# Kernel optimization log

Measured on AMD Instinct MI355X. Metric: run time of the kernel, lower is better.

## Reference

```python
import jax, jax.numpy as jnp
import numpy as np

H = 16  # num_heads

def setup_inputs() -> dict:
    key = jax.random.key(0)
    ks = jax.random.split(key, 9)
    B, S, D = 4, 1024, 1024
    s = 0.02
    return {
        "x": jax.random.normal(ks[0], (B, S, D), jnp.float32),
        "Wq": jax.random.normal(ks[1], (D, D), jnp.float32) * s,
        "bq": jax.random.normal(ks[2], (D,), jnp.float32) * s,
        "Wk": jax.random.normal(ks[3], (D, D), jnp.float32) * s,
        "bk": jax.random.normal(ks[4], (D,), jnp.float32) * s,
        "Wv": jax.random.normal(ks[5], (D, D), jnp.float32) * s,
        "bv": jax.random.normal(ks[6], (D,), jnp.float32) * s,
        "Wo": jax.random.normal(ks[7], (D, D), jnp.float32) * s,
        "bo": jax.random.normal(ks[8], (D,), jnp.float32) * s,
    }

def reference(x, Wq, bq, Wk, bk, Wv, bv, Wo, bo):
    B, S, D = x.shape
    hd = D // H
    # Batched equivalent of the per-head Linear loop: project then split into heads.
    def proj(W, b):
        return (x @ W + b).reshape(B, S, H, hd).transpose(0, 2, 1, 3)  # [B,H,S,hd]
    q, k, v = proj(Wq, bq), proj(Wk, bk), proj(Wv, bv)
    scores = jnp.einsum("bhqd,bhkd->bhqk", q, k) / jnp.sqrt(jnp.float32(hd))
    probs = jax.nn.softmax(scores, axis=-1)  # [B,H,S,S] (dropout p=0 -> identity)
    ctx = jnp.einsum("bhqk,bhkd->bhqd", probs, v)  # [B,H,S,hd]
    ctx = ctx.transpose(0, 2, 1, 3).reshape(B, S, D)  # concat heads
    out = ctx @ Wo + bo
    return out, probs
```

## Files before the change

### kernel.cpp

```cpp
#include <hip/hip_runtime.h>
#include <math.h>

typedef unsigned short u16;
typedef __attribute__((ext_vector_type(8))) short short8;
typedef __attribute__((ext_vector_type(4))) float f32x4;

#define BB 4
#define SS 1024
#define DD 1024
#define NH 16
#define HD 64
#define BH 64

__device__ __forceinline__ u16 f2bf(float f) {
    union { float f; unsigned u; } v;
    v.f = f;
    unsigned r = v.u + 0x7fffu + ((v.u >> 16) & 1u);
    return (u16)(r >> 16);
}

__global__ void cast_bf16(const float* __restrict__ X, u16* __restrict__ Y) {
    const int i = blockIdx.x * blockDim.x + threadIdx.x;
    const float4 v = reinterpret_cast<const float4*>(X)[i];
    ushort4 o;
    o.x = f2bf(v.x); o.y = f2bf(v.y); o.z = f2bf(v.z); o.w = f2bf(v.w);
    reinterpret_cast<ushort4*>(Y)[i] = o;
}

__global__ void transpose_cast_w(const float* __restrict__ W0, const float* __restrict__ W1,
                                 const float* __restrict__ W2, const float* __restrict__ W3,
                                 u16* __restrict__ O0, u16* __restrict__ O1,
                                 u16* __restrict__ O2, u16* __restrict__ O3) {
    __shared__ float T[64][65];
    const int z = blockIdx.z;
    const float* W = (z == 0) ? W0 : (z == 1) ? W1 : (z == 2) ? W2 : W3;
    u16* O = (z == 0) ? O0 : (z == 1) ? O1 : (z == 2) ? O2 : O3;
    const int k0 = blockIdx.x * 64, n0 = blockIdx.y * 64;
    const int x = threadIdx.x & 63, yq = threadIdx.x >> 6;
#pragma unroll
    for (int r = 0; r < 16; r++) {
        const int row = yq * 16 + r;
        T[row][x] = W[(size_t)(k0 + row) * 1024 + n0 + x];
    }
    __syncthreads();
#pragma unroll
    for (int r = 0; r < 16; r++) {
        const int row = yq * 16 + r;
        O[(size_t)(n0 + row) * 1024 + k0 + x] = f2bf(T[x][row]);
    }
}

__global__ void transpose_v(const u16* __restrict__ V, u16* __restrict__ VT) {
    __shared__ u16 T[64][66];
    const int t0 = blockIdx.x * 64;
    const size_t hbase = (size_t)blockIdx.y * (SS * HD);
    const int x = threadIdx.x & 63, yq = threadIdx.x >> 6;
#pragma unroll
    for (int r = 0; r < 16; r++) {
        const int trow = yq * 16 + r;
        T[trow][x] = V[hbase + (size_t)(t0 + trow) * 64 + x];
    }
    __syncthreads();
#pragma unroll
    for (int r = 0; r < 16; r++) {
        const int drow = yq * 16 + r;
        VT[hbase + (size_t)drow * 1024 + t0 + x] = T[x][drow];
    }
}

template <int MODE, int QKV>
__global__ __launch_bounds__(256) void mfma_gemm(
    const u16* __restrict__ A,
    const u16* __restrict__ Bt0, const u16* __restrict__ Bt1, const u16* __restrict__ Bt2,
    const float* __restrict__ bias0, const float* __restrict__ bias1, const float* __restrict__ bias2,
    void* __restrict__ out0, void* __restrict__ out1, void* __restrict__ out2) {
    __shared__ __align__(16) u16 As[128][32];
    __shared__ __align__(16) u16 Bs[128][32];

    const u16* Bt = Bt0;
    const float* bias = bias0;
    void* out = out0;
    if (QKV) {
        const int z = blockIdx.z;
        Bt = (z == 0) ? Bt0 : (z == 1) ? Bt1 : Bt2;
        bias = (z == 0) ? bias0 : (z == 1) ? bias1 : bias2;
        out = (z == 0) ? out0 : (z == 1) ? out1 : out2;
    }

    const int tid = threadIdx.x;
    const int w = tid >> 6, lane = tid & 63, l15 = lane & 15, quad = lane >> 4;
    const int wr = w >> 1, wc = w & 1;
    const int m0 = blockIdx.y * 128, n0 = blockIdx.x * 128;

    f32x4 acc[4][4];
#pragma unroll
    for (int i = 0; i < 4; i++)
#pragma unroll
        for (int j = 0; j < 4; j++) acc[i][j] = (f32x4){0.f, 0.f, 0.f, 0.f};

    for (int k0 = 0; k0 < 1024; k0 += 32) {
#pragma unroll
        for (int i = 0; i < 2; i++) {
            const int c = i * 256 + tid;
            const int row = c >> 2, in4 = c & 3;
            *(uint4*)(&As[row][in4 * 8]) =
                *(const uint4*)(A + (size_t)(m0 + row) * 1024 + k0 + in4 * 8);
            *(uint4*)(&Bs[row][in4 * 8]) =
                *(const uint4*)(Bt + (size_t)(n0 + row) * 1024 + k0 + in4 * 8);
        }
        __syncthreads();
        short8 af[4], bf[4];
#pragma unroll
        for (int i = 0; i < 4; i++)
            af[i] = *(const short8*)(&As[wr * 64 + i * 16 + l15][quad * 8]);
#pragma unroll
        for (int j = 0; j < 4; j++)
            bf[j] = *(const short8*)(&Bs[wc * 64 + j * 16 + l15][quad * 8]);
#pragma unroll
        for (int i = 0; i < 4; i++)
#pragma unroll
            for (int j = 0; j < 4; j++)
                acc[i][j] = __builtin_amdgcn_mfma_f32_16x16x32_bf16(af[i], bf[j], acc[i][j], 0, 0, 0);
        __syncthreads();
    }

#pragma unroll
    for (int i = 0; i < 4; i++) {
#pragma unroll
        for (int j = 0; j < 4; j++) {
            const int nn = n0 + wc * 64 + j * 16 + l15;
            const float bb = bias[nn];
#pragma unroll
            for (int r = 0; r < 4; r++) {
                const int mm = m0 + wr * 64 + i * 16 + quad * 4 + r;
                const float val = acc[i][j][r] + bb;
                if (MODE == 0) {
                    const int b = mm >> 10, s = mm & 1023, h = nn >> 6, d = nn & 63;
                    ((u16*)out)[((size_t)(b * NH + h) * SS + s) * HD + d] = f2bf(val);
                } else {
                    ((float*)out)[(size_t)mm * 1024 + nn] = val;
                }
            }
        }
    }
}

__global__ __launch_bounds__(256) void attn_fused(
    const u16* __restrict__ Qg, const u16* __restrict__ Kg, const u16* __restrict__ VTg,
    float* __restrict__ probs, u16* __restrict__ ctx) {
    __shared__ __align__(16) u16 Qs[2][64][32];
    __shared__ __align__(16) u16 Ks[2][64][32];
    __shared__ __align__(16) u16 Vs[2][64][32];
    __shared__ __align__(16) u16 Ps[4][2][16][32];

    const int tid = threadIdx.x;
    const int w = tid >> 6, lane = tid & 63, l15 = lane & 15, quad = lane >> 4;
    const int s0 = blockIdx.x * 64;
    const int bh = blockIdx.y;
    const size_t hbase = (size_t)bh * (SS * HD);

#pragma unroll
    for (int i = 0; i < 2; i++) {
        const int c = i * 256 + tid;
        const int row = c >> 3, ch = c & 7;
        *(uint4*)(&Qs[ch >> 2][row][(ch & 3) * 8]) =
            *(const uint4*)(Qg + hbase + (size_t)(s0 + row) * 64 + ch * 8);
    }

    float m_i[4], l_i[4];
#pragma unroll
    for (int r = 0; r < 4; r++) { m_i[r] = -1e30f; l_i[r] = 0.f; }

#pragma unroll 1
    for (int kt = 0; kt < 16; kt++) {
#pragma unroll
        for (int i = 0; i < 2; i++) {
            const int c = i * 256 + tid;
            const int row = c >> 3, ch = c & 7;
            *(uint4*)(&Ks[ch >> 2][row][(ch & 3) * 8]) =
                *(const uint4*)(Kg + hbase + (size_t)(kt * 64 + row) * 64 + ch * 8);
        }
        __syncthreads();
        const short8 aq0 = *(const short8*)(&Qs[0][w * 16 + l15][quad * 8]);
        const short8 aq1 = *(const short8*)(&Qs[1][w * 16 + l15][quad * 8]);
        f32x4 sc[4];
#pragma unroll
        for (int c = 0; c < 4; c++) {
            const short8 bk0 = *(const short8*)(&Ks[0][c * 16 + l15][quad * 8]);
            const short8 bk1 = *(const short8*)(&Ks[1][c * 16 + l15][quad * 8]);
            f32x4 z = {0.f, 0.f, 0.f, 0.f};
            z = __builtin_amdgcn_mfma_f32_16x16x32_bf16(aq0, bk0, z, 0, 0, 0);
            z = __builtin_amdgcn_mfma_f32_16x16x32_bf16(aq1, bk1, z, 0, 0, 0);
            sc[c] = z;
        }
#pragma unroll
        for (int r = 0; r < 4; r++) {
            float v = fmaxf(fmaxf(sc[0][r], sc[1][r]), fmaxf(sc[2][r], sc[3][r])) * 0.125f;
            v = fmaxf(v, __shfl_xor(v, 1));
            v = fmaxf(v, __shfl_xor(v, 2));
            v = fmaxf(v, __shfl_xor(v, 4));
            v = fmaxf(v, __shfl_xor(v, 8));
            const float mn = fmaxf(m_i[r], v);
            float ss = 0.f;
#pragma unroll
            for (int c = 0; c < 4; c++) ss += __expf(sc[c][r] * 0.125f - mn);
            ss += __shfl_xor(ss, 1);
            ss += __shfl_xor(ss, 2);
            ss += __shfl_xor(ss, 4);
            ss += __shfl_xor(ss, 8);
            l_i[r] = l_i[r] * __expf(m_i[r] - mn) + ss;
            m_i[r] = mn;
        }
        __syncthreads();
    }

    float linv[4];
#pragma unroll
    for (int r = 0; r < 4; r++) linv[r] = 1.0f / l_i[r];

    f32x4 oacc[4];
#pragma unroll
    for (int j = 0; j < 4; j++) oacc[j] = (f32x4){0.f, 0.f, 0.f, 0.f};

#pragma unroll 1
    for (int kt = 0; kt < 16; kt++) {
#pragma unroll
        for (int i = 0; i < 2; i++) {
            const int c = i * 256 + tid;
            const int row = c >> 3, ch = c & 7;
            *(uint4*)(&Ks[ch >> 2][row][(ch & 3) * 8]) =
                *(const uint4*)(Kg + hbase + (size_t)(kt * 64 + row) * 64 + ch * 8);
            *(uint4*)(&Vs[ch >> 2][row][(ch & 3) * 8]) =
                *(const uint4*)(VTg + hbase + (size_t)row * 1024 + kt * 64 + ch * 8);
        }
        __syncthreads();
        const short8 aq0 = *(const short8*)(&Qs[0][w * 16 + l15][quad * 8]);
        const short8 aq1 = *(const short8*)(&Qs[1][w * 16 + l15][quad * 8]);
        f32x4 sc[4];
#pragma unroll
        for (int c = 0; c < 4; c++) {
            const short8 bk0 = *(const short8*)(&Ks[0][c * 16 + l15][quad * 8]);
            const short8 bk1 = *(const short8*)(&Ks[1][c * 16 + l15][quad * 8]);
            f32x4 z = {0.f, 0.f, 0.f, 0.f};
            z = __builtin_amdgcn_mfma_f32_16x16x32_bf16(aq0, bk0, z, 0, 0, 0);
            z = __builtin_amdgcn_mfma_f32_16x16x32_bf16(aq1, bk1, z, 0, 0, 0);
            sc[c] = z;
        }
        const int qrow = s0 + w * 16 + quad * 4;
#pragma unroll
        for (int c = 0; c < 4; c++) {
            const int t = kt * 64 + c * 16 + l15;
#pragma unroll
            for (int r = 0; r < 4; r++) {
                const float p = __expf(sc[c][r] * 0.125f - m_i[r]) * linv[r];
                probs[((size_t)bh * SS + (qrow + r)) * SS + t] = p;
                Ps[w][c >> 1][quad * 4 + r][(c & 1) * 16 + l15] = f2bf(p);
            }
        }
        const short8 ap0 = *(const short8*)(&Ps[w][0][l15][quad * 8]);
        const short8 ap1 = *(const short8*)(&Ps[w][1][l15][quad * 8]);
#pragma unroll
        for (int j = 0; j < 4; j++) {
            const short8 bv0 = *(const short8*)(&Vs[0][j * 16 + l15][quad * 8]);
            const short8 bv1 = *(const short8*)(&Vs[1][j * 16 + l15][quad * 8]);
            oacc[j] = __builtin_amdgcn_mfma_f32_16x16x32_bf16(ap0, bv0, oacc[j], 0, 0, 0);
            oacc[j] = __builtin_amdgcn_mfma_f32_16x16x32_bf16(ap1, bv1, oacc[j], 0, 0, 0);
        }
        __syncthreads();
    }

    const int b = bh >> 4, h = bh & 15;
#pragma unroll
    for (int j = 0; j < 4; j++)
#pragma unroll
        for (int r = 0; r < 4; r++) {
            const int s = s0 + w * 16 + quad * 4 + r;
            ctx[((size_t)b * SS + s) * DD + h * HD + j * 16 + l15] = f2bf(oacc[j][r]);
        }
}

extern "C" void kernel_launch(void* const* d_in, const int* in_sizes, int n_in,
                              void* d_out, int out_size, void* d_ws, size_t ws_size,
                              hipStream_t stream) {
    const float* x  = (const float*)d_in[0];
    const float* Wq = (const float*)d_in[1];
    const float* bq = (const float*)d_in[2];
    const float* Wk = (const float*)d_in[3];
    const float* bk = (const float*)d_in[4];
    const float* Wv = (const float*)d_in[5];
    const float* bv = (const float*)d_in[6];
    const float* Wo = (const float*)d_in[7];
    const float* bo = (const float*)d_in[8];

    float* out   = (float*)d_out;
    float* probs = out + (size_t)BB * SS * DD;

    char* ws = (char*)d_ws;
    u16* xb   = (u16*)(ws);
    u16* Wtq  = (u16*)(ws + (8ull << 20));
    u16* Wtk  = (u16*)(ws + (10ull << 20));
    u16* Wtv  = (u16*)(ws + (12ull << 20));
    u16* Wto  = (u16*)(ws + (14ull << 20));
    u16* qb   = (u16*)(ws + (16ull << 20));
    u16* kb   = (u16*)(ws + (24ull << 20));
    u16* vb   = (u16*)(ws + (32ull << 20));
    u16* vTb  = (u16*)(ws + (40ull << 20));
    u16* ctxb = (u16*)(ws + (48ull << 20));

    const dim3 blk(256);

    cast_bf16<<<dim3(4096), blk, 0, stream>>>(x, xb);
    transpose_cast_w<<<dim3(16, 16, 4), blk, 0, stream>>>(Wq, Wk, Wv, Wo, Wtq, Wtk, Wtv, Wto);

    mfma_gemm<0, 1><<<dim3(8, 32, 3), blk, 0, stream>>>(
        xb, Wtq, Wtk, Wtv, bq, bk, bv, qb, kb, vb);

    transpose_v<<<dim3(16, 64), blk, 0, stream>>>(vb, vTb);

    attn_fused<<<dim3(16, 64), blk, 0, stream>>>(qb, kb, vTb, probs, ctxb);

    mfma_gemm<1, 0><<<dim3(8, 32), blk, 0, stream>>>(
        ctxb, Wto, nullptr, nullptr, bo, nullptr, nullptr, out, nullptr, nullptr);
}
```

Before: 470.2 us.

## Use direct global-to-LDS loads and transposed score layout for vectorized prob stores

The projection GEMM now uses global_load_lds to stream A and B tiles straight into LDS, with the K step doubled to 64 and two MFMA k-slices per step. The attention kernel swaps the MFMA operand order (K as A, Q as B) so each lane owns one query row. That lets the softmax reductions use cross-quad shuffles only and lets probs be written as contiguous float4 stores. The first pass reads K straight from global memory without LDS or barriers, and Q is kept in registers instead of LDS. The aim is to cut LDS staging, barriers and the cost of scattered scalar probability writes, at the risk of uncoalesced K reads in pass one and LDS layout mismatches from global_load_lds.

```diff
diff --git a/kernel.cpp b/kernel.cpp
--- a/kernel.cpp
+++ b/kernel.cpp
@@ -17,6 +17,11 @@
     v.f = f;
     unsigned r = v.u + 0x7fffu + ((v.u >> 16) & 1u);
     return (u16)(r >> 16);
+}
+
+__device__ __forceinline__ void gll16(const void* g, void* l) {
+    __builtin_amdgcn_global_load_lds((__attribute__((address_space(1))) void*)g,
+                                     (__attribute__((address_space(3))) void*)l, 16, 0, 0);
 }
 
 __global__ void cast_bf16(const float* __restrict__ X, u16* __restrict__ Y) {
@@ -74,8 +79,8 @@
     const u16* __restrict__ Bt0, const u16* __restrict__ Bt1, const u16* __restrict__ Bt2,
     const float* __restrict__ bias0, const float* __restrict__ bias1, const float* __restrict__ bias2,
     void* __restrict__ out0, void* __restrict__ out1, void* __restrict__ out2) {
-    __shared__ __align__(16) u16 As[128][32];
-    __shared__ __align__(16) u16 Bs[128][32];
+    __shared__ __align__(16) u16 As[128][64];
+    __shared__ __align__(16) u16 Bs[128][64];
 
     const u16* Bt = Bt0;
     const float* bias = bias0;
@@ -92,35 +97,40 @@
     const int wr = w >> 1, wc = w & 1;
     const int m0 = blockIdx.y * 128, n0 = blockIdx.x * 128;
 
+    const int srow = tid >> 3, sch = tid & 7;
+    const u16* Ag = A + (size_t)(m0 + srow) * 1024 + sch * 8;
+    const u16* Bg = Bt + (size_t)(n0 + srow) * 1024 + sch * 8;
+
     f32x4 acc[4][4];
 #pragma unroll
     for (int i = 0; i < 4; i++)
 #pragma unroll
         for (int j = 0; j < 4; j++) acc[i][j] = (f32x4){0.f, 0.f, 0.f, 0.f};
 
-    for (int k0 = 0; k0 < 1024; k0 += 32) {
-#pragma unroll
-        for (int i = 0; i < 2; i++) {
-            const int c = i * 256 + tid;
-            const int row = c >> 2, in4 = c & 3;
-            *(uint4*)(&As[row][in4 * 8]) =
-                *(const uint4*)(A + (size_t)(m0 + row) * 1024 + k0 + in4 * 8);
-            *(uint4*)(&Bs[row][in4 * 8]) =
-                *(const uint4*)(Bt + (size_t)(n0 + row) * 1024 + k0 + in4 * 8);
+    for (int k0 = 0; k0 < 1024; k0 += 64) {
+#pragma unroll
+        for (int i = 0; i < 4; i++) {
+            gll16(Ag + (size_t)(i * 32) * 1024 + k0, &As[i * 32 + w * 8][0]);
+            gll16(Bg + (size_t)(i * 32) * 1024 + k0, &Bs[i * 32 + w * 8][0]);
         }
         __syncthreads();
-        short8 af[4], bf[4];
+        short8 af[2][4], bf[2][4];
+#pragma unroll
+        for (int ks = 0; ks < 2; ks++) {
+#pragma unroll
+            for (int i = 0; i < 4; i++)
+                af[ks][i] = *(const short8*)(&As[wr * 64 + i * 16 + l15][ks * 32 + quad * 8]);
+#pragma unroll
+            for (int j = 0; j < 4; j++)
+                bf[ks][j] = *(const short8*)(&Bs[wc * 64 + j * 16 + l15][ks * 32 + quad * 8]);
+        }
 #pragma unroll
         for (int i = 0; i < 4; i++)
-            af[i] = *(const short8*)(&As[wr * 64 + i * 16 + l15][quad * 8]);
-#pragma unroll
-        for (int j = 0; j < 4; j++)
-            bf[j] = *(const short8*)(&Bs[wc * 64 + j * 16 + l15][quad * 8]);
-#pragma unroll
-        for (int i = 0; i < 4; i++)
-#pragma unroll
-            for (int j = 0; j < 4; j++)
-                acc[i][j] = __builtin_amdgcn_mfma_f32_16x16x32_bf16(af[i], bf[j], acc[i][j], 0, 0, 0);
+#pragma unroll
+            for (int j = 0; j < 4; j++) {
+                acc[i][j] = __builtin_amdgcn_mfma_f32_16x16x32_bf16(af[0][i], bf[0][j], acc[i][j], 0, 0, 0);
+                acc[i][j] = __builtin_amdgcn_mfma_f32_16x16x32_bf16(af[1][i], bf[1][j], acc[i][j], 0, 0, 0);
+            }
         __syncthreads();
     }
 
@@ -148,7 +158,6 @@
 __global__ __launch_bounds__(256) void attn_fused(
     const u16* __restrict__ Qg, const u16* __restrict__ Kg, const u16* __restrict__ VTg,
     float* __restrict__ probs, u16* __restrict__ ctx) {
-    __shared__ __align__(16) u16 Qs[2][64][32];
     __shared__ __align__(16) u16 Ks[2][64][32];
     __shared__ __align__(16) u16 Vs[2][64][32];
     __shared__ __align__(16) u16 Ps[4][2][16][32];
@@ -159,103 +168,91 @@
     const int bh = blockIdx.y;
     const size_t hbase = (size_t)bh * (SS * HD);
 
-#pragma unroll
-    for (int i = 0; i < 2; i++) {
-        const int c = i * 256 + tid;
-        const int row = c >> 3, ch = c & 7;
-        *(uint4*)(&Qs[ch >> 2][row][(ch & 3) * 8]) =
-            *(const uint4*)(Qg + hbase + (size_t)(s0 + row) * 64 + ch * 8);
-    }
-
-    float m_i[4], l_i[4];
-#pragma unroll
-    for (int r = 0; r < 4; r++) { m_i[r] = -1e30f; l_i[r] = 0.f; }
-
+    const int qg = s0 + w * 16 + l15;
+    const short8 bq0 = *(const short8*)(Qg + hbase + (size_t)qg * 64 + quad * 8);
+    const short8 bq1 = *(const short8*)(Qg + hbase + (size_t)qg * 64 + 32 + quad * 8);
+
+    float m_i = -1e30f, l_i = 0.f;
 #pragma unroll 1
     for (int kt = 0; kt < 16; kt++) {
+        f32x4 sc[4];
+#pragma unroll
+        for (int c = 0; c < 4; c++) {
+            const u16* kr = Kg + hbase + (size_t)(kt * 64 + c * 16 + l15) * 64 + quad * 8;
+            const short8 ak0 = *(const short8*)kr;
+            const short8 ak1 = *(const short8*)(kr + 32);
+            f32x4 z = {0.f, 0.f, 0.f, 0.f};
+            z = __builtin_amdgcn_mfma_f32_16x16x32_bf16(ak0, bq0, z, 0, 0, 0);
+            z = __builtin_amdgcn_mfma_f32_16x16x32_bf16(ak1, bq1, z, 0, 0, 0);
+            sc[c] = z;
+        }
+        float vm = -1e30f;
+#pragma unroll
+        for (int c = 0; c < 4; c++)
+#pragma unroll
+            for (int r = 0; r < 4; r++) {
+                sc[c][r] *= 0.125f;
+                vm = fmaxf(vm, sc[c][r]);
+            }
+        vm = fmaxf(vm, __shfl_xor(vm, 16));
+        vm = fmaxf(vm, __shfl_xor(vm, 32));
+        const float mn = fmaxf(m_i, vm);
+        float ss = 0.f;
+#pragma unroll
+        for (int c = 0; c < 4; c++)
+#pragma unroll
+            for (int r = 0; r < 4; r++) ss += __expf(sc[c][r] - mn);
+        ss += __shfl_xor(ss, 16);
+        ss += __shfl_xor(ss, 32);
+        l_i = l_i * __expf(m_i - mn) + ss;
+        m_i = mn;
+    }
+    const float linv = 1.0f / l_i;
+
+    f32x4 oacc[4];
+#pragma unroll
+    for (int j = 0; j < 4; j++) oacc[j] = (f32x4){0.f, 0.f, 0.f, 0.f};
+
+    const size_t prow = ((size_t)bh * SS + qg) * SS;
+
+#pragma unroll 1
+    for (int kt = 0; kt < 16; kt++) {
 #pragma unroll
         for (int i = 0; i < 2; i++) {
             const int c = i * 256 + tid;
-            const int row = c >> 3, ch = c & 7;
-            *(uint4*)(&Ks[ch >> 2][row][(ch & 3) * 8]) =
-                *(const uint4*)(Kg + hbase + (size_t)(kt * 64 + row) * 64 + ch * 8);
+            const int ks = c >> 8, row = (c >> 2) & 63, ch = c & 3;
+            const int cb = i * 256 + (tid & ~63);
+            gll16(Kg + hbase + (size_t)(kt * 64 + row) * 64 + ks * 32 + ch * 8,
+                  &Ks[0][0][0] + (size_t)cb * 8);
+            gll16(VTg + hbase + (size_t)row * 1024 + kt * 64 + ks * 32 + ch * 8,
+                  &Vs[0][0][0] + (size_t)cb * 8);
         }
         __syncthreads();
-        const short8 aq0 = *(const short8*)(&Qs[0][w * 16 + l15][quad * 8]);
-        const short8 aq1 = *(const short8*)(&Qs[1][w * 16 + l15][quad * 8]);
+
         f32x4 sc[4];
 #pragma unroll
         for (int c = 0; c < 4; c++) {
-            const short8 bk0 = *(const short8*)(&Ks[0][c * 16 + l15][quad * 8]);
-            const short8 bk1 = *(const short8*)(&Ks[1][c * 16 + l15][quad * 8]);
+            const short8 ak0 = *(const short8*)(&Ks[0][c * 16 + l15][quad * 8]);
+            const short8 ak1 = *(const short8*)(&Ks[1][c * 16 + l15][quad * 8]);
             f32x4 z = {0.f, 0.f, 0.f, 0.f};
-            z = __builtin_amdgcn_mfma_f32_16x16x32_bf16(aq0, bk0, z, 0, 0, 0);
-            z = __builtin_amdgcn_mfma_f32_16x16x32_bf16(aq1, bk1, z, 0, 0, 0);
+            z = __builtin_amdgcn_mfma_f32_16x16x32_bf16(ak0, bq0, z, 0, 0, 0);
+            z = __builtin_amdgcn_mfma_f32_16x16x32_bf16(ak1, bq1, z, 0, 0, 0);
             sc[c] = z;
         }
 #pragma unroll
-        for (int r = 0; r < 4; r++) {
-            float v = fmaxf(fmaxf(sc[0][r], sc[1][r]), fmaxf(sc[2][r], sc[3][r])) * 0.125f;
-            v = fmaxf(v, __shfl_xor(v, 1));
-            v = fmaxf(v, __shfl_xor(v, 2));
-            v = fmaxf(v, __shfl_xor(v, 4));
-            v = fmaxf(v, __shfl_xor(v, 8));
-            const float mn = fmaxf(m_i[r], v);
-            float ss = 0.f;
-#pragma unroll
-            for (int c = 0; c < 4; c++) ss += __expf(sc[c][r] * 0.125f - mn);
-            ss += __shfl_xor(ss, 1);
-            ss += __shfl_xor(ss, 2);
-            ss += __shfl_xor(ss, 4);
-            ss += __shfl_xor(ss, 8);
-            l_i[r] = l_i[r] * __expf(m_i[r] - mn) + ss;
-            m_i[r] = mn;
-        }
-        __syncthreads();
-    }
-
-    float linv[4];
-#pragma unroll
-    for (int r = 0; r < 4; r++) linv[r] = 1.0f / l_i[r];
-
-    f32x4 oacc[4];
-#pragma unroll
-    for (int j = 0; j < 4; j++) oacc[j] = (f32x4){0.f, 0.f, 0.f, 0.f};
-
-#pragma unroll 1
-    for (int kt = 0; kt < 16; kt++) {
-#pragma unroll
-        for (int i = 0; i < 2; i++) {
-            const int c = i * 256 + tid;
-            const int row = c >> 3, ch = c & 7;
-            *(uint4*)(&Ks[ch >> 2][row][(ch & 3) * 8]) =
-                *(const uint4*)(Kg + hbase + (size_t)(kt * 64 + row) * 64 + ch * 8);
-            *(uint4*)(&Vs[ch >> 2][row][(ch & 3) * 8]) =
-                *(const uint4*)(VTg + hbase + (size_t)row * 1024 + kt * 64 + ch * 8);
-        }
-        __syncthreads();
-        const short8 aq0 = *(const short8*)(&Qs[0][w * 16 + l15][quad * 8]);
-        const short8 aq1 = *(const short8*)(&Qs[1][w * 16 + l15][quad * 8]);
-        f32x4 sc[4];
-#pragma unroll
         for (int c = 0; c < 4; c++) {
-            const short8 bk0 = *(const short8*)(&Ks[0][c * 16 + l15][quad * 8]);
-            const short8 bk1 = *(const short8*)(&Ks[1][c * 16 + l15][quad * 8]);
-            f32x4 z = {0.f, 0.f, 0.f, 0.f};
-            z = __builtin_amdgcn_mfma_f32_16x16x32_bf16(aq0, bk0, z, 0, 0, 0);
-            z = __builtin_amdgcn_mfma_f32_16x16x32_bf16(aq1, bk1, z, 0, 0, 0);
-            sc[c] = z;
-        }
-        const int qrow = s0 + w * 16 + quad * 4;
-#pragma unroll
-        for (int c = 0; c < 4; c++) {
-            const int t = kt * 64 + c * 16 + l15;
+            float p[4];
+            f32x4 pv;
 #pragma unroll
             for (int r = 0; r < 4; r++) {
-                const float p = __expf(sc[c][r] * 0.125f - m_i[r]) * linv[r];
-                probs[((size_t)bh * SS + (qrow + r)) * SS + t] = p;
-                Ps[w][c >> 1][quad * 4 + r][(c & 1) * 16 + l15] = f2bf(p);
+                p[r] = __expf(sc[c][r] * 0.125f - m_i) * linv;
+                pv[r] = p[r];
             }
+            *(f32x4*)(probs + prow + kt * 64 + c * 16 + quad * 4) = pv;
+            uint2 pk;
+            pk.x = (unsigned)f2bf(p[0]) | ((unsigned)f2bf(p[1]) << 16);
+            pk.y = (unsigned)f2bf(p[2]) | ((unsigned)f2bf(p[3]) << 16);
+            *(uint2*)(&Ps[w][c >> 1][l15][(c & 1) * 16 + quad * 4]) = pk;
         }
         const short8 ap0 = *(const short8*)(&Ps[w][0][l15][quad * 8]);
         const short8 ap1 = *(const short8*)(&Ps[w][1][l15][quad * 8]);
```

After: 492.5 us. +4.7%, slower.
